# Kernel tuning notes

Hardware: AMD Instinct MI355X
Metric: run time of the kernel (lower is better)

The kernel has to match this reference:

```python
import jax, jax.numpy as jnp
import numpy as np

N_NODES = 20000
N_EDGES = 320000
NFEAT = 50
ALPHA = 0.2  # leaky relu slope
EPS = 1e-16


def _gat_head(x, src, dst, W, a, concat):
    # x: (N, Fin), W: (Fin, Fout), a: (2*Fout,)
    N = x.shape[0]
    Wh = x @ W                      # (N, Fout)
    Fout = W.shape[1]
    # edge_h @ a == Wh[src] @ a[:Fout] + Wh[dst] @ a[Fout:]
    s_src = Wh @ a[:Fout]           # (N,)
    s_dst = Wh @ a[Fout:]           # (N,)
    e = jax.nn.leaky_relu(s_src[src] + s_dst[dst], negative_slope=ALPHA)  # (E,)
    # segment softmax over incoming edges of each target node
    e_max = jax.ops.segment_max(e, dst, num_segments=N)   # (N,)
    e_exp = jnp.exp(e - e_max[dst])                         # (E,)
    e_sum = jax.ops.segment_sum(e_exp, dst, num_segments=N)
    att = e_exp / (e_sum[dst] + EPS)                        # (E,)
    msg = Wh[src] * att[:, None]                            # (E, Fout)
    h = jax.ops.segment_sum(msg, dst, num_segments=N)       # (N, Fout)
    return jax.nn.elu(h) if concat else h


def _multi_head(x, src, dst, W, a, concat):
    # W: (H, Fin, Fout), a: (H, 2*Fout) -> (H, N, Fout)
    return jax.vmap(_gat_head, in_axes=(None, None, None, 0, 0, None))(x, src, dst, W, a, concat)


def setup_inputs() -> dict:
    key = jax.random.key(0)
    ks = jax.random.split(key, 8)
    x = jax.random.normal(ks[0], (N_NODES, NFEAT), dtype=jnp.float32)
    edge_index = jax.random.randint(ks[1], (2, N_EDGES), 0, N_NODES, dtype=jnp.int64)
    s = 0.1
    W1 = jax.random.normal(ks[2], (4, NFEAT, 256), dtype=jnp.float32) * s
    a1 = jax.random.normal(ks[3], (4, 512), dtype=jnp.float32) * s
    W2 = jax.random.normal(ks[4], (4, 1024, 256), dtype=jnp.float32) * s
    a2 = jax.random.normal(ks[5], (4, 512), dtype=jnp.float32) * s
    W3 = jax.random.normal(ks[6], (6, 1024, 121), dtype=jnp.float32) * s
    a3 = jax.random.normal(ks[7], (6, 242), dtype=jnp.float32) * s
    return {"x": x, "edge_index": edge_index, "W1": W1, "a1": a1, "W2": W2, "a2": a2, "W3": W3, "a3": a3}


def reference(x, edge_index, W1, a1, W2, a2, W3, a3):
    src, dst = edge_index[0], edge_index[1]
    N = x.shape[0]
    # layer 1: 4 heads, concat -> (N, 1024), then elu
    h1 = _multi_head(x, src, dst, W1, a1, True)      # (4, N, 256)
    x1 = jnp.transpose(h1, (1, 0, 2)).reshape(N, -1)  # concat along feature dim
    x1 = jax.nn.elu(x1)
    # layer 2: 4 heads, concat + skip connection, then elu
    h2 = _multi_head(x1, src, dst, W2, a2, True)
    x2 = jnp.transpose(h2, (1, 0, 2)).reshape(N, -1)
    x2 = jax.nn.elu(x2 + x1)
    # layer 3: 6 heads, no concat-elu, mean over heads
    h3 = _multi_head(x2, src, dst, W3, a3, False)     # (6, N, 121)
    x3 = jnp.mean(h3, axis=0)
    return jax.nn.sigmoid(x3)
```

## Files before the change

### kernel.cpp

```cpp
#include <hip/hip_runtime.h>
#include <cstdint>

#define N_NODES 20000
#define N_EDGES 320000
#define ALPHA 0.2f
#define GAT_EPS 1e-16f
#define MPAD 20096
#define RBLK 157
#define RHI 20
#define SCAN_BLKS 80
#define BT_ROWS 1152

typedef __attribute__((ext_vector_type(8))) _Float16 half8;
typedef __attribute__((ext_vector_type(4))) _Float16 half4t;
typedef __attribute__((ext_vector_type(16))) float f32x16;
typedef __attribute__((ext_vector_type(2))) float f32x2;

__device__ __forceinline__ float elu1(float x) { return x > 0.f ? x : __expf(x) - 1.f; }

__device__ __forceinline__ unsigned char f2fp8(float x) {
    return (unsigned char)(__builtin_amdgcn_cvt_pk_fp8_f32(x, 0.f, 0, false) & 0xff);
}

__device__ __forceinline__ void async16(const void* g, void* l) {
    __builtin_amdgcn_global_load_lds(
        (const __attribute__((address_space(1))) unsigned int*)g,
        (__attribute__((address_space(3))) unsigned int*)l, 16, 0, 0);
}

__device__ __forceinline__ float rdlanef(float v, int j) {
    return __int_as_float(__builtin_amdgcn_readlane(__float_as_int(v), j));
}

__global__ void hist_kernel(const int* __restrict__ dst, int* __restrict__ counts, int E) {
    int e = blockIdx.x * blockDim.x + threadIdx.x;
    if (e < E) atomicAdd(&counts[dst[e]], 1);
}

__global__ void scan1_kernel(const int* __restrict__ counts, int* __restrict__ excl,
                             int* __restrict__ partial, int N) {
    __shared__ int sh[256];
    int t = threadIdx.x, b = blockIdx.x;
    int i = b * 256 + t;
    int v = (i < N) ? counts[i] : 0;
    sh[t] = v;
    __syncthreads();
    for (int d = 1; d < 256; d <<= 1) {
        int x = (t >= d) ? sh[t - d] : 0;
        __syncthreads();
        sh[t] += x;
        __syncthreads();
    }
    if (i < N) excl[i] = sh[t] - v;
    if (t == 255) partial[b] = sh[255];
}

__global__ void scan2_kernel(int* __restrict__ partial) {
    __shared__ int sh[128];
    int t = threadIdx.x;
    int v = (t < SCAN_BLKS) ? partial[t] : 0;
    sh[t] = v;
    __syncthreads();
    for (int d = 1; d < 128; d <<= 1) {
        int x = (t >= d) ? sh[t - d] : 0;
        __syncthreads();
        sh[t] += x;
        __syncthreads();
    }
    if (t < SCAN_BLKS) partial[t] = sh[t] - v;
}

__global__ void scan3_kernel(const int* __restrict__ excl, const int* __restrict__ partial,
                             int* __restrict__ rowptr, int* __restrict__ cursor, int N, int E) {
    int t = threadIdx.x, b = blockIdx.x;
    int i = b * 256 + t;
    if (i < N) {
        int v = excl[i] + partial[b];
        rowptr[i] = v;
        cursor[i] = v;
    }
    if (i == 0) rowptr[N] = E;
}

__global__ void scatter_kernel(const int* __restrict__ src, const int* __restrict__ dst,
                               int* __restrict__ cursor, int* __restrict__ esrc, int E) {
    int e = blockIdx.x * blockDim.x + threadIdx.x;
    if (e < E) {
        int p = atomicAdd(&cursor[dst[e]], 1);
        esrc[p] = src[e];
    }
}

__global__ void pack_x16(const float* __restrict__ x, _Float16* __restrict__ A) {
    int idx = blockIdx.x * 256 + threadIdx.x;
    int r = idx >> 6, c = idx & 63;
    float v = (r < N_NODES && c < 50) ? x[r * 50 + c] : 0.f;
    A[idx] = (_Float16)v;
}

__global__ void pack_bt1(const float* __restrict__ W, _Float16* __restrict__ Bt) {
    int idx = blockIdx.x * 256 + threadIdx.x;
    int c = idx >> 6, k = idx & 63;
    int h = c >> 8, f = c & 255;
    float v = (k < 50) ? W[((size_t)h * 50 + k) * 256 + f] : 0.f;
    Bt[idx] = (_Float16)v;
}

__global__ void pack_bt16(const float* __restrict__ W, _Float16* __restrict__ Bt,
                          int F, int Fpad, int Ctot) {
    int c = blockIdx.y;
    int k = blockIdx.x * blockDim.x + threadIdx.x;
    float v = 0.f;
    if (c < Ctot) {
        int h = c / Fpad, f = c - h * Fpad;
        if (f < F) v = W[(size_t)h * 1024 * F + (size_t)k * F + f];
    }
    Bt[(size_t)c * 1024 + k] = (_Float16)v;
}

__global__ __launch_bounds__(64) void wtilde_kernel(const float* __restrict__ W,
                                                    const float* __restrict__ a,
                                                    _Float16* __restrict__ BT, int Kreal,
                                                    int Kdim, int F, int H, int Nfeat) {
    int k = blockIdx.x, j = blockIdx.y;
    if (j >= 2 * H) return;
    int lane = threadIdx.x;
    int h = j < H ? j : j - H;
    int ao = j < H ? 0 : F;
    float s = 0.f;
    if (k < Kreal) {
        const float* wp = W + ((size_t)h * Kreal + k) * F;
        const float* ap = a + (size_t)h * 2 * F + ao;
        for (int f = lane; f < F; f += 64) s += wp[f] * ap[f];
    }
#pragma unroll
    for (int off = 32; off; off >>= 1) s += __shfl_down(s, off);
    if (lane == 0) BT[(size_t)(Nfeat + j) * Kdim + k] = (_Float16)s;
}

__global__ __launch_bounds__(256) void gemm_f16(const _Float16* __restrict__ A,
                                                const _Float16* __restrict__ BT,
                                                unsigned char* __restrict__ C8,
                                                float* __restrict__ SPRE,
                                                int M, int Nfeat, int ld, int Kdim, int Cblk) {
    int id = blockIdx.x;
    int xm = id & 7, q = id >> 3;
    int cb = q % Cblk, rh = q / Cblk;
    int rb = rh * 8 + xm;
    if (rb >= RBLK) return;
    __shared__ __align__(16) _Float16 sA[128 * 64];
    __shared__ __align__(16) _Float16 sB[128 * 64];
    int t = threadIdx.x;
    int row0 = rb * 128, col0 = cb * 128;
    int lane = t & 63, wave = t >> 6;
    int wm = wave >> 1, wn = wave & 1;
    int l31 = lane & 31;
    int lhi = lane >> 5;

    const _Float16* gA = A + (size_t)row0 * Kdim;
    const _Float16* gB = BT + (size_t)col0 * Kdim;

    int sR[4], sgl[4];
#pragma unroll
    for (int i = 0; i < 4; i++) {
        int m = i * 256 + t;
        sR[i] = m >> 3;
        sgl[i] = (m & 7) ^ (sR[i] & 7);
    }

    f32x16 acc[2][2] = {};

    for (int k0 = 0; k0 < Kdim; k0 += 64) {
        __syncthreads();
#pragma unroll
        for (int i = 0; i < 4; i++) {
            const _Float16* pa = gA + (size_t)sR[i] * Kdim + k0 + sgl[i] * 8;
            const _Float16* pb = gB + (size_t)sR[i] * Kdim + k0 + sgl[i] * 8;
            async16(pa, sA + (i * 256 + t) * 8);
            async16(pb, sB + (i * 256 + t) * 8);
        }
        __syncthreads();
#pragma unroll
        for (int kk = 0; kk < 4; kk++) {
            int g = kk * 2 + lhi;
            half8 af[2], bf[2];
#pragma unroll
            for (int mt = 0; mt < 2; mt++) {
                int R = wm * 64 + mt * 32 + l31;
                int gp = g ^ (R & 7);
                af[mt] = *(const half8*)(sA + R * 64 + gp * 8);
            }
#pragma unroll
            for (int nt = 0; nt < 2; nt++) {
                int R = wn * 64 + nt * 32 + l31;
                int gp = g ^ (R & 7);
                bf[nt] = *(const half8*)(sB + R * 64 + gp * 8);
            }
#pragma unroll
            for (int mt = 0; mt < 2; mt++)
#pragma unroll
                for (int nt = 0; nt < 2; nt++)
                    acc[mt][nt] = __builtin_amdgcn_mfma_f32_32x32x16_f16(af[mt], bf[nt], acc[mt][nt], 0, 0, 0);
        }
    }

    int cb32 = col0 + wn * 64 + l31;
    int rb32 = row0 + wm * 64 + 4 * lhi;
#pragma unroll
    for (int mt = 0; mt < 2; mt++)
#pragma unroll
        for (int nt = 0; nt < 2; nt++) {
            int gc = cb32 + nt * 32;
            if (gc < Nfeat) {
#pragma unroll
                for (int r = 0; r < 16; r++) {
                    int gr = rb32 + mt * 32 + (r & 3) + 8 * (r >> 2);
                    if (gr < M) C8[(size_t)gr * ld + gc] = f2fp8(acc[mt][nt][r]);
                }
            } else if (gc < Nfeat + 12) {
                int j = gc - Nfeat;
#pragma unroll
                for (int r = 0; r < 16; r++) {
                    int gr = rb32 + mt * 32 + (r & 3) + 8 * (r >> 2);
                    if (gr < M) SPRE[(size_t)j * N_NODES + gr] = acc[mt][nt][r];
                }
            }
        }
}

__global__ __launch_bounds__(256) void attagg256_kernel(const int* __restrict__ rowptr,
                                                        const int* __restrict__ esrc,
                                                        const float* __restrict__ SPRE,
                                                        const unsigned char* __restrict__ WH8,
                                                        _Float16* __restrict__ X16,
                                                        int use_skip, int N) {
    int n = blockIdx.x;
    int h = threadIdx.x >> 6;
    int lane = threadIdx.x & 63;
    int start = rowptr[n], end = rowptr[n + 1];
    int cnt = end - start;
    const float* ss = SPRE + (size_t)h * N;
    float sd = SPRE[(size_t)(4 + h) * N + n];
    const unsigned char* Wb = WH8 + h * 256 + lane * 4;
    float a0 = 0.f, a1 = 0.f, a2 = 0.f, a3 = 0.f;

    if (cnt <= 64) {
        int e = start + lane;
        bool act = e < end;
        int idx = act ? esrc[e] : 0;

        unsigned int wA[8], wB[8], wC[8], wD[8];
        auto ISSUE = [&](unsigned int (&buf)[8], int base) {
#pragma unroll
            for (int u = 0; u < 8; u++) {
                int ij = __builtin_amdgcn_readlane(idx, base + u);
                buf[u] = *(const unsigned int*)(Wb + ((size_t)(unsigned)ij << 10));
            }
        };
        ISSUE(wA, 0);
        if (cnt > 8)  ISSUE(wB, 8);
        if (cnt > 16) ISSUE(wC, 16);
        if (cnt > 24) ISSUE(wD, 24);

        float sc = -1e30f;
        if (act) {
            sc = ss[idx] + sd;
            sc = sc > 0.f ? sc : ALPHA * sc;
        }
        float m = sc;
#pragma unroll
        for (int off = 1; off < 64; off <<= 1) m = fmaxf(m, __shfl_xor(m, off));
        float ptil = act ? __expf(sc - m) : 0.f;
        float s = ptil;
#pragma unroll
        for (int off = 1; off < 64; off <<= 1) s += __shfl_xor(s, off);
        float p = ptil * (1.f / (s + GAT_EPS));

        auto CONSUME = [&](unsigned int (&buf)[8], int base) {
#pragma unroll
            for (int u = 0; u < 8; u++) {
                float pj = rdlanef(p, base + u);
                f32x2 lo = __builtin_amdgcn_cvt_pk_f32_fp8((int)buf[u], false);
                f32x2 hi = __builtin_amdgcn_cvt_pk_f32_fp8((int)buf[u], true);
                a0 += pj * lo.x; a1 += pj * lo.y; a2 += pj * hi.x; a3 += pj * hi.y;
            }
        };
        CONSUME(wA, 0);
        if (cnt > 8)  { if (cnt > 32) ISSUE(wA, 32); CONSUME(wB, 8); }
        if (cnt > 16) { if (cnt > 40) ISSUE(wB, 40); CONSUME(wC, 16); }
        if (cnt > 24) { if (cnt > 48) ISSUE(wC, 48); CONSUME(wD, 24); }
        if (cnt > 32) { if (cnt > 56) ISSUE(wD, 56); CONSUME(wA, 32); }
        if (cnt > 40) CONSUME(wB, 40);
        if (cnt > 48) CONSUME(wC, 48);
        if (cnt > 56) CONSUME(wD, 56);
    } else {
        float m = -1e30f, s = 0.f;
        int sidx = 0; float ssc = -1e30f;
        for (int e0 = start; e0 < end; e0 += 64) {
            int e = e0 + lane;
            bool act = e < end;
            int idx = act ? esrc[e] : 0;
            float sc = -1e30f;
            if (act) {
                sc = ss[idx] + sd;
                sc = sc > 0.f ? sc : ALPHA * sc;
            }
            sidx = idx; ssc = sc;
            float mn = fmaxf(m, sc);
            s = s * __expf(m - mn) + (act ? __expf(sc - mn) : 0.f);
            m = mn;
        }
        float lm = m;
#pragma unroll
        for (int off = 1; off < 64; off <<= 1) m = fmaxf(m, __shfl_xor(m, off));
        float ptil = s * __expf(lm - m);
        s = ptil;
#pragma unroll
        for (int off = 1; off < 64; off <<= 1) s += __shfl_xor(s, off);
        float inv = 1.f / (s + GAT_EPS);

        int lastStart = start + (((end - start - 1) >> 6) << 6);
        for (int e0 = start; e0 < end; e0 += 64) {
            int e = e0 + lane;
            bool act = e < end;
            int idx; float p;
            if (e0 == lastStart) {
                idx = sidx;
                p = act ? __expf(ssc - m) * inv : 0.f;
            } else {
                idx = act ? esrc[e] : 0;
                float sc = -1e30f;
                if (act) {
                    sc = ss[idx] + sd;
                    sc = sc > 0.f ? sc : ALPHA * sc;
                }
                p = act ? __expf(sc - m) * inv : 0.f;
            }
            int cn = end - e0; if (cn > 64) cn = 64;
            int j = 0;
            for (; j + 4 <= cn; j += 4) {
                int i0 = __builtin_amdgcn_readlane(idx, j);
                int i1 = __builtin_amdgcn_readlane(idx, j + 1);
                int i2 = __builtin_amdgcn_readlane(idx, j + 2);
                int i3 = __builtin_amdgcn_readlane(idx, j + 3);
                float p0 = rdlanef(p, j), p1 = rdlanef(p, j + 1);
                float p2 = rdlanef(p, j + 2), p3 = rdlanef(p, j + 3);
                unsigned int w0 = *(const unsigned int*)(Wb + (size_t)i0 * 1024);
                unsigned int w1 = *(const unsigned int*)(Wb + (size_t)i1 * 1024);
                unsigned int w2 = *(const unsigned int*)(Wb + (size_t)i2 * 1024);
                unsigned int w3 = *(const unsigned int*)(Wb + (size_t)i3 * 1024);
                f32x2 l0 = __builtin_amdgcn_cvt_pk_f32_fp8((int)w0, false);
                f32x2 h0v = __builtin_amdgcn_cvt_pk_f32_fp8((int)w0, true);
                f32x2 l1 = __builtin_amdgcn_cvt_pk_f32_fp8((int)w1, false);
                f32x2 h1v = __builtin_amdgcn_cvt_pk_f32_fp8((int)w1, true);
                f32x2 l2 = __builtin_amdgcn_cvt_pk_f32_fp8((int)w2, false);
                f32x2 h2v = __builtin_amdgcn_cvt_pk_f32_fp8((int)w2, true);
                f32x2 l3 = __builtin_amdgcn_cvt_pk_f32_fp8((int)w3, false);
                f32x2 h3v = __builtin_amdgcn_cvt_pk_f32_fp8((int)w3, true);
                a0 += p0 * l0.x + p1 * l1.x + p2 * l2.x + p3 * l3.x;
                a1 += p0 * l0.y + p1 * l1.y + p2 * l2.y + p3 * l3.y;
                a2 += p0 * h0v.x + p1 * h1v.x + p2 * h2v.x + p3 * h3v.x;
                a3 += p0 * h0v.y + p1 * h1v.y + p2 * h2v.y + p3 * h3v.y;
            }
            for (; j < cn; j++) {
                int ij = __builtin_amdgcn_readlane(idx, j);
                float pj = rdlanef(p, j);
                unsigned int w = *(const unsigned int*)(Wb + (size_t)ij * 1024);
                f32x2 lo = __builtin_amdgcn_cvt_pk_f32_fp8((int)w, false);
                f32x2 hi = __builtin_amdgcn_cvt_pk_f32_fp8((int)w, true);
                a0 += pj * lo.x; a1 += pj * lo.y; a2 += pj * hi.x; a3 += pj * hi.y;
            }
        }
    }

    size_t o = (size_t)n * 1024 + h * 256 + lane * 4;
    float v0, v1, v2, v3;
    if (use_skip) {
        half4t sk = *(const half4t*)(X16 + o);
        v0 = elu1(elu1(a0) + (float)sk.x);
        v1 = elu1(elu1(a1) + (float)sk.y);
        v2 = elu1(elu1(a2) + (float)sk.z);
        v3 = elu1(elu1(a3) + (float)sk.w);
    } else {
        v0 = elu1(elu1(a0)); v1 = elu1(elu1(a1));
        v2 = elu1(elu1(a2)); v3 = elu1(elu1(a3));
    }
    half4t r;
    r.x = (_Float16)v0; r.y = (_Float16)v1; r.z = (_Float16)v2; r.w = (_Float16)v3;
    *(half4t*)(X16 + o) = r;
}

__global__ __launch_bounds__(384) void attagg726_kernel(const int* __restrict__ rowptr,
                                                        const int* __restrict__ esrc,
                                                        const float* __restrict__ SPRE,
                                                        const unsigned char* __restrict__ WH8,
                                                        float* __restrict__ out, int N) {
    __shared__ float part[6][124];
    int n = blockIdx.x;
    int t = threadIdx.x;
    int h = t >> 6;
    int lane = t & 63;
    int start = rowptr[n], end = rowptr[n + 1];
    int cnt = end - start;
    const float* ss = SPRE + (size_t)h * N;
    float sd = SPRE[(size_t)(6 + h) * N + n];
    const unsigned char* Wb = WH8 + h * 124 + 2 * lane;
    float a0 = 0.f, a1 = 0.f;

    if (cnt <= 64) {
        int e = start + lane;
        bool act = e < end;
        int idx = act ? esrc[e] : 0;

        unsigned short wA[8], wB[8], wC[8], wD[8];
        auto ISSUE = [&](unsigned short (&buf)[8], int base) {
#pragma unroll
            for (int u = 0; u < 8; u++) {
                int ij = __builtin_amdgcn_readlane(idx, base + u);
                buf[u] = *(const unsigned short*)(Wb + (size_t)(unsigned)ij * 768u);
            }
        };
        ISSUE(wA, 0);
        if (cnt > 8)  ISSUE(wB, 8);
        if (cnt > 16) ISSUE(wC, 16);
        if (cnt > 24) ISSUE(wD, 24);

        float sc = -1e30f;
        if (act) {
            sc = ss[idx] + sd;
            sc = sc > 0.f ? sc : ALPHA * sc;
        }
        float m = sc;
#pragma unroll
        for (int off = 1; off < 64; off <<= 1) m = fmaxf(m, __shfl_xor(m, off));
        float ptil = act ? __expf(sc - m) : 0.f;
        float s = ptil;
#pragma unroll
        for (int off = 1; off < 64; off <<= 1) s += __shfl_xor(s, off);
        float p = ptil * (1.f / (s + GAT_EPS));

        auto CONSUME = [&](unsigned short (&buf)[8], int base) {
#pragma unroll
            for (int u = 0; u < 8; u++) {
                float pj = rdlanef(p, base + u);
                f32x2 f = __builtin_amdgcn_cvt_pk_f32_fp8((int)buf[u], false);
                a0 += pj * f.x; a1 += pj * f.y;
            }
        };
        CONSUME(wA, 0);
        if (cnt > 8)  { if (cnt > 32) ISSUE(wA, 32); CONSUME(wB, 8); }
        if (cnt > 16) { if (cnt > 40) ISSUE(wB, 40); CONSUME(wC, 16); }
        if (cnt > 24) { if (cnt > 48) ISSUE(wC, 48); CONSUME(wD, 24); }
        if (cnt > 32) { if (cnt > 56) ISSUE(wD, 56); CONSUME(wA, 32); }
        if (cnt > 40) CONSUME(wB, 40);
        if (cnt > 48) CONSUME(wC, 48);
        if (cnt > 56) CONSUME(wD, 56);
    } else {
        float m = -1e30f, s = 0.f;
        int sidx = 0; float ssc = -1e30f;
        for (int e0 = start; e0 < end; e0 += 64) {
            int e = e0 + lane;
            bool act = e < end;
            int idx = act ? esrc[e] : 0;
            float sc = -1e30f;
            if (act) {
                sc = ss[idx] + sd;
                sc = sc > 0.f ? sc : ALPHA * sc;
            }
            sidx = idx; ssc = sc;
            float mn = fmaxf(m, sc);
            s = s * __expf(m - mn) + (act ? __expf(sc - mn) : 0.f);
            m = mn;
        }
        float lm = m;
#pragma unroll
        for (int off = 1; off < 64; off <<= 1) m = fmaxf(m, __shfl_xor(m, off));
        float ptil = s * __expf(lm - m);
        s = ptil;
#pragma unroll
        for (int off = 1; off < 64; off <<= 1) s += __shfl_xor(s, off);
        float inv = 1.f / (s + GAT_EPS);

        int lastStart = start + (((end - start - 1) >> 6) << 6);
        for (int e0 = start; e0 < end; e0 += 64) {
            int e = e0 + lane;
            bool act = e < end;
            int idx; float p;
            if (e0 == lastStart) {
                idx = sidx;
                p = act ? __expf(ssc - m) * inv : 0.f;
            } else {
                idx = act ? esrc[e] : 0;
                float sc = -1e30f;
                if (act) {
                    sc = ss[idx] + sd;
                    sc = sc > 0.f ? sc : ALPHA * sc;
                }
                p = act ? __expf(sc - m) * inv : 0.f;
            }
            int cn = end - e0; if (cn > 64) cn = 64;
            int j = 0;
            for (; j + 4 <= cn; j += 4) {
                int i0 = __builtin_amdgcn_readlane(idx, j);
                int i1 = __builtin_amdgcn_readlane(idx, j + 1);
                int i2 = __builtin_amdgcn_readlane(idx, j + 2);
                int i3 = __builtin_amdgcn_readlane(idx, j + 3);
                float p0 = rdlanef(p, j), p1 = rdlanef(p, j + 1);
                float p2 = rdlanef(p, j + 2), p3 = rdlanef(p, j + 3);
                unsigned short w0 = *(const unsigned short*)(Wb + (size_t)i0 * 768);
                unsigned short w1 = *(const unsigned short*)(Wb + (size_t)i1 * 768);
                unsigned short w2 = *(const unsigned short*)(Wb + (size_t)i2 * 768);
                unsigned short w3 = *(const unsigned short*)(Wb + (size_t)i3 * 768);
                f32x2 f0 = __builtin_amdgcn_cvt_pk_f32_fp8((int)w0, false);
                f32x2 f1 = __builtin_amdgcn_cvt_pk_f32_fp8((int)w1, false);
                f32x2 f2 = __builtin_amdgcn_cvt_pk_f32_fp8((int)w2, false);
                f32x2 f3 = __builtin_amdgcn_cvt_pk_f32_fp8((int)w3, false);
                a0 += p0 * f0.x + p1 * f1.x + p2 * f2.x + p3 * f3.x;
                a1 += p0 * f0.y + p1 * f1.y + p2 * f2.y + p3 * f3.y;
            }
            for (; j < cn; j++) {
                int ij = __builtin_amdgcn_readlane(idx, j);
                float pj = rdlanef(p, j);
                unsigned short w = *(const unsigned short*)(Wb + (size_t)ij * 768);
                f32x2 f = __builtin_amdgcn_cvt_pk_f32_fp8((int)w, false);
                a0 += pj * f.x; a1 += pj * f.y;
            }
        }
    }

    if (lane < 62) {
        part[h][2 * lane]     = a0;
        part[h][2 * lane + 1] = a1;
    }
    __syncthreads();
    if (t < 121) {
        float tot = (part[0][t] + part[1][t] + part[2][t] +
                     part[3][t] + part[4][t] + part[5][t]) * (1.f / 6.f);
        out[(size_t)n * 121 + t] = 1.f / (1.f + __expf(-tot));
    }
}

extern "C" void kernel_launch(void* const* d_in, const int* in_sizes, int n_in,
                              void* d_out, int out_size, void* d_ws, size_t ws_size,
                              hipStream_t stream) {
    const float* x  = (const float*)d_in[0];
    const int*   ei = (const int*)d_in[1];
    const float* W1 = (const float*)d_in[2];
    const float* a1 = (const float*)d_in[3];
    const float* W2 = (const float*)d_in[4];
    const float* a2 = (const float*)d_in[5];
    const float* W3 = (const float*)d_in[6];
    const float* a3 = (const float*)d_in[7];
    float* out = (float*)d_out;
    const int N = N_NODES, E = N_EDGES;
    const int* src = ei;
    const int* dst = ei + E;

    char* ws = (char*)d_ws;
    size_t off = 0;
    auto alloc = [&](size_t b) { size_t o = off; off += (b + 255) & ~(size_t)255; return o; };
    _Float16* X16  = (_Float16*)(ws + alloc((size_t)MPAD * 1024 * 2));
    unsigned char* WH8 = (unsigned char*)(ws + alloc((size_t)MPAD * 1024));
    _Float16* BT16 = (_Float16*)(ws + alloc((size_t)BT_ROWS * 1024 * 2));
    _Float16* A1   = (_Float16*)(ws + alloc((size_t)MPAD * 64 * 2));
    _Float16* BT1  = (_Float16*)(ws + alloc((size_t)BT_ROWS * 64 * 2));
    float* SPRE   = (float*)(ws + alloc((size_t)12 * N * 4));
    int*   rowptr = (int*)(ws + alloc((size_t)(N + 1) * 4));
    int*   cursor = (int*)(ws + alloc((size_t)N * 4));
    int*   counts = (int*)(ws + alloc((size_t)N * 4));
    int*   excl   = (int*)(ws + alloc((size_t)N * 4));
    int*   partial= (int*)(ws + alloc((size_t)SCAN_BLKS * 4));
    int*   esrc   = (int*)(ws + alloc((size_t)E * 4));

    hipMemsetAsync(counts, 0, (size_t)N * 4, stream);
    hist_kernel<<<(E + 255) / 256, 256, 0, stream>>>(dst, counts, E);
    scan1_kernel<<<SCAN_BLKS, 256, 0, stream>>>(counts, excl, partial, N);
    scan2_kernel<<<1, 128, 0, stream>>>(partial);
    scan3_kernel<<<SCAN_BLKS, 256, 0, stream>>>(excl, partial, rowptr, cursor, N, E);
    scatter_kernel<<<(E + 255) / 256, 256, 0, stream>>>(src, dst, cursor, esrc, E);
    hipMemsetAsync(X16 + (size_t)N * 1024, 0, (size_t)(MPAD - N) * 1024 * 2, stream);

    pack_x16<<<MPAD * 64 / 256, 256, 0, stream>>>(x, A1);
    pack_bt1<<<1024 * 64 / 256, 256, 0, stream>>>(W1, BT1);
    wtilde_kernel<<<dim3(64, 8), 64, 0, stream>>>(W1, a1, BT1, 50, 64, 256, 4, 1024);
    gemm_f16<<<8 * RHI * 9, 256, 0, stream>>>(A1, BT1, WH8, SPRE, N, 1024, 1024, 64, 9);
    attagg256_kernel<<<N, 256, 0, stream>>>(rowptr, esrc, SPRE, WH8, X16, 0, N);

    pack_bt16<<<dim3(4, 1024), 256, 0, stream>>>(W2, BT16, 256, 256, 1024);
    wtilde_kernel<<<dim3(1024, 8), 64, 0, stream>>>(W2, a2, BT16, 1024, 1024, 256, 4, 1024);
    gemm_f16<<<8 * RHI * 9, 256, 0, stream>>>(X16, BT16, WH8, SPRE, N, 1024, 1024, 1024, 9);
    attagg256_kernel<<<N, 256, 0, stream>>>(rowptr, esrc, SPRE, WH8, X16, 1, N);

    pack_bt16<<<dim3(4, 744), 256, 0, stream>>>(W3, BT16, 121, 124, 744);
    wtilde_kernel<<<dim3(1024, 12), 64, 0, stream>>>(W3, a3, BT16, 1024, 1024, 121, 6, 744);
    gemm_f16<<<8 * RHI * 6, 256, 0, stream>>>(X16, BT16, WH8, SPRE, N, 744, 768, 1024, 6);
    attagg726_kernel<<<N, 384, 0, stream>>>(rowptr, esrc, SPRE, WH8, out, N);
}
```

Baseline: 444.5 us.

## Aggregate raw input features before projection in layer one (reassociate GEMM)

Layer one now computes only the attention scores with a small GEMM, then aggregates the 64-wide fp16 input rows per head (aggx1) instead of gathering 1024-wide fp8 projected rows. A second GEMM multiplies the aggregated features by W1 per head, using a per-column-block K offset, and applies the double ELU in its epilogue, writing fp16 X16 directly. This cuts layer-one gather traffic and the fp8 round-trip of Wh. In exchange it adds an extra GEMM launch, a new 256-wide intermediate buffer, and a changed precision path.

```diff
diff --git a/kernel.cpp b/kernel.cpp
--- a/kernel.cpp
+++ b/kernel.cpp
@@ -142,7 +142,8 @@
                                                 const _Float16* __restrict__ BT,
                                                 unsigned char* __restrict__ C8,
                                                 float* __restrict__ SPRE,
-                                                int M, int Nfeat, int ld, int Kdim, int Cblk) {
+                                                int M, int Nfeat, int ld, int Kdim, int Cblk,
+                                                int ldA, int mode) {
     int id = blockIdx.x;
     int xm = id & 7, q = id >> 3;
     int cb = q % Cblk, rh = q / Cblk;
@@ -157,7 +158,8 @@
     int l31 = lane & 31;
     int lhi = lane >> 5;
 
-    const _Float16* gA = A + (size_t)row0 * Kdim;
+    int koff = (mode == 1) ? ((cb >> 1) * 64) : 0;
+    const _Float16* gA = A + (size_t)row0 * ldA + koff;
     const _Float16* gB = BT + (size_t)col0 * Kdim;
 
     int sR[4], sgl[4];
@@ -174,7 +176,7 @@
         __syncthreads();
 #pragma unroll
         for (int i = 0; i < 4; i++) {
-            const _Float16* pa = gA + (size_t)sR[i] * Kdim + k0 + sgl[i] * 8;
+            const _Float16* pa = gA + (size_t)sR[i] * ldA + k0 + sgl[i] * 8;
             const _Float16* pb = gB + (size_t)sR[i] * Kdim + k0 + sgl[i] * 8;
             async16(pa, sA + (i * 256 + t) * 8);
             async16(pb, sB + (i * 256 + t) * 8);
@@ -206,6 +208,23 @@
 
     int cb32 = col0 + wn * 64 + l31;
     int rb32 = row0 + wm * 64 + 4 * lhi;
+    if (mode == 1) {
+        _Float16* C16 = (_Float16*)C8;
+#pragma unroll
+        for (int mt = 0; mt < 2; mt++)
+#pragma unroll
+            for (int nt = 0; nt < 2; nt++) {
+                int gc = cb32 + nt * 32;
+                if (gc < Nfeat) {
+#pragma unroll
+                    for (int r = 0; r < 16; r++) {
+                        int gr = rb32 + mt * 32 + (r & 3) + 8 * (r >> 2);
+                        if (gr < M) C16[(size_t)gr * ld + gc] = (_Float16)elu1(elu1(acc[mt][nt][r]));
+                    }
+                }
+            }
+        return;
+    }
 #pragma unroll
     for (int mt = 0; mt < 2; mt++)
 #pragma unroll
@@ -228,12 +247,11 @@
         }
 }
 
-__global__ __launch_bounds__(256) void attagg256_kernel(const int* __restrict__ rowptr,
-                                                        const int* __restrict__ esrc,
-                                                        const float* __restrict__ SPRE,
-                                                        const unsigned char* __restrict__ WH8,
-                                                        _Float16* __restrict__ X16,
-                                                        int use_skip, int N) {
+__global__ __launch_bounds__(256) void aggx1_kernel(const int* __restrict__ rowptr,
+                                                    const int* __restrict__ esrc,
+                                                    const float* __restrict__ SPRE,
+                                                    const _Float16* __restrict__ A1,
+                                                    _Float16* __restrict__ XB, int N) {
     int n = blockIdx.x;
     int h = threadIdx.x >> 6;
     int lane = threadIdx.x & 63;
@@ -241,20 +259,21 @@
     int cnt = end - start;
     const float* ss = SPRE + (size_t)h * N;
     float sd = SPRE[(size_t)(4 + h) * N + n];
-    const unsigned char* Wb = WH8 + h * 256 + lane * 4;
-    float a0 = 0.f, a1 = 0.f, a2 = 0.f, a3 = 0.f;
+    const unsigned char* Wb = (const unsigned char*)A1 + 2 * lane;
+    float acc = 0.f;
 
     if (cnt <= 64) {
         int e = start + lane;
         bool act = e < end;
         int idx = act ? esrc[e] : 0;
-
-        unsigned int wA[8], wB[8], wC[8], wD[8];
-        auto ISSUE = [&](unsigned int (&buf)[8], int base) {
+        int voff = idx << 7;
+
+        unsigned short wA[8], wB[8], wC[8], wD[8];
+        auto ISSUE = [&](unsigned short (&buf)[8], int base) {
 #pragma unroll
             for (int u = 0; u < 8; u++) {
-                int ij = __builtin_amdgcn_readlane(idx, base + u);
-                buf[u] = *(const unsigned int*)(Wb + ((size_t)(unsigned)ij << 10));
+                int off = __builtin_amdgcn_readlane(voff, base + u);
+                buf[u] = *(const unsigned short*)(Wb + (unsigned)off);
             }
         };
         ISSUE(wA, 0);
@@ -276,13 +295,11 @@
         for (int off = 1; off < 64; off <<= 1) s += __shfl_xor(s, off);
         float p = ptil * (1.f / (s + GAT_EPS));
 
-        auto CONSUME = [&](unsigned int (&buf)[8], int base) {
+        auto CONSUME = [&](unsigned short (&buf)[8], int base) {
 #pragma unroll
             for (int u = 0; u < 8; u++) {
                 float pj = rdlanef(p, base + u);
-                f32x2 lo = __builtin_amdgcn_cvt_pk_f32_fp8((int)buf[u], false);
-                f32x2 hi = __builtin_amdgcn_cvt_pk_f32_fp8((int)buf[u], true);
-                a0 += pj * lo.x; a1 += pj * lo.y; a2 += pj * hi.x; a3 += pj * hi.y;
+                acc += pj * (float)(*(const _Float16*)&buf[u]);
             }
         };
         CONSUME(wA, 0);
@@ -337,87 +354,45 @@
                 p = act ? __expf(sc - m) * inv : 0.f;
             }
             int cn = end - e0; if (cn > 64) cn = 64;
-            int j = 0;
-            for (; j + 4 <= cn; j += 4) {
-                int i0 = __builtin_amdgcn_readlane(idx, j);
-                int i1 = __builtin_amdgcn_readlane(idx, j + 1);
-                int i2 = __builtin_amdgcn_readlane(idx, j + 2);
-                int i3 = __builtin_amdgcn_readlane(idx, j + 3);
-                float p0 = rdlanef(p, j), p1 = rdlanef(p, j + 1);
-                float p2 = rdlanef(p, j + 2), p3 = rdlanef(p, j + 3);
-                unsigned int w0 = *(const unsigned int*)(Wb + (size_t)i0 * 1024);
-                unsigned int w1 = *(const unsigned int*)(Wb + (size_t)i1 * 1024);
-                unsigned int w2 = *(const unsigned int*)(Wb + (size_t)i2 * 1024);
-                unsigned int w3 = *(const unsigned int*)(Wb + (size_t)i3 * 1024);
-                f32x2 l0 = __builtin_amdgcn_cvt_pk_f32_fp8((int)w0, false);
-                f32x2 h0v = __builtin_amdgcn_cvt_pk_f32_fp8((int)w0, true);
-                f32x2 l1 = __builtin_amdgcn_cvt_pk_f32_fp8((int)w1, false);
-                f32x2 h1v = __builtin_amdgcn_cvt_pk_f32_fp8((int)w1, true);
-                f32x2 l2 = __builtin_amdgcn_cvt_pk_f32_fp8((int)w2, false);
-                f32x2 h2v = __builtin_amdgcn_cvt_pk_f32_fp8((int)w2, true);
-                f32x2 l3 = __builtin_amdgcn_cvt_pk_f32_fp8((int)w3, false);
-                f32x2 h3v = __builtin_amdgcn_cvt_pk_f32_fp8((int)w3, true);
-                a0 += p0 * l0.x + p1 * l1.x + p2 * l2.x + p3 * l3.x;
-                a1 += p0 * l0.y + p1 * l1.y + p2 * l2.y + p3 * l3.y;
-                a2 += p0 * h0v.x + p1 * h1v.x + p2 * h2v.x + p3 * h3v.x;
-                a3 += p0 * h0v.y + p1 * h1v.y + p2 * h2v.y + p3 * h3v.y;
-            }
-            for (; j < cn; j++) {
+            for (int j = 0; j < cn; j++) {
                 int ij = __builtin_amdgcn_readlane(idx, j);
                 float pj = rdlanef(p, j);
-                unsigned int w = *(const unsigned int*)(Wb + (size_t)ij * 1024);
-                f32x2 lo = __builtin_amdgcn_cvt_pk_f32_fp8((int)w, false);
-                f32x2 hi = __builtin_amdgcn_cvt_pk_f32_fp8((int)w, true);
-                a0 += pj * lo.x; a1 += pj * lo.y; a2 += pj * hi.x; a3 += pj * hi.y;
-            }
-        }
-    }
-
-    size_t o = (size_t)n * 1024 + h * 256 + lane * 4;
-    float v0, v1, v2, v3;
-    if (use_skip) {
-        half4t sk = *(const half4t*)(X16 + o);
-        v0 = elu1(elu1(a0) + (float)sk.x);
-        v1 = elu1(elu1(a1) + (float)sk.y);
-        v2 = elu1(elu1(a2) + (float)sk.z);
-        v3 = elu1(elu1(a3) + (float)sk.w);
-    } else {
-        v0 = elu1(elu1(a0)); v1 = elu1(elu1(a1));
-        v2 = elu1(elu1(a2)); v3 = elu1(elu1(a3));
-    }
-    half4t r;
-    r.x = (_Float16)v0; r.y = (_Float16)v1; r.z = (_Float16)v2; r.w = (_Float16)v3;
-    *(half4t*)(X16 + o) = r;
-}
-
-__global__ __launch_bounds__(384) void attagg726_kernel(const int* __restrict__ rowptr,
+                unsigned short w = *(const unsigned short*)(Wb + ((size_t)(unsigned)ij << 7));
+                acc += pj * (float)(*(const _Float16*)&w);
+            }
+        }
+    }
+
+    XB[(size_t)n * 256 + h * 64 + lane] = (_Float16)acc;
+}
+
+__global__ __launch_bounds__(256) void attagg256_kernel(const int* __restrict__ rowptr,
                                                         const int* __restrict__ esrc,
                                                         const float* __restrict__ SPRE,
                                                         const unsigned char* __restrict__ WH8,
-                                                        float* __restrict__ out, int N) {
-    __shared__ float part[6][124];
+                                                        _Float16* __restrict__ X16,
+                                                        int use_skip, int N) {
     int n = blockIdx.x;
-    int t = threadIdx.x;
-    int h = t >> 6;
-    int lane = t & 63;
+    int h = threadIdx.x >> 6;
+    int lane = threadIdx.x & 63;
     int start = rowptr[n], end = rowptr[n + 1];
     int cnt = end - start;
     const float* ss = SPRE + (size_t)h * N;
-    float sd = SPRE[(size_t)(6 + h) * N + n];
-    const unsigned char* Wb = WH8 + h * 124 + 2 * lane;
-    float a0 = 0.f, a1 = 0.f;
+    float sd = SPRE[(size_t)(4 + h) * N + n];
+    const unsigned char* Wb = WH8 + h * 256 + lane * 4;
+    float a0 = 0.f, a1 = 0.f, a2 = 0.f, a3 = 0.f;
 
     if (cnt <= 64) {
         int e = start + lane;
         bool act = e < end;
         int idx = act ? esrc[e] : 0;
 
-        unsigned short wA[8], wB[8], wC[8], wD[8];
-        auto ISSUE = [&](unsigned short (&buf)[8], int base) {
+        unsigned int wA[8], wB[8], wC[8], wD[8];
+        auto ISSUE = [&](unsigned int (&buf)[8], int base) {
 #pragma unroll
             for (int u = 0; u < 8; u++) {
                 int ij = __builtin_amdgcn_readlane(idx, base + u);
-                buf[u] = *(const unsigned short*)(Wb + (size_t)(unsigned)ij * 768u);
+                buf[u] = *(const unsigned int*)(Wb + ((size_t)(unsigned)ij << 10));
             }
         };
         ISSUE(wA, 0);
@@ -439,12 +414,13 @@
         for (int off = 1; off < 64; off <<= 1) s += __shfl_xor(s, off);
         float p = ptil * (1.f / (s + GAT_EPS));
 
-        auto CONSUME = [&](unsigned short (&buf)[8], int base) {
+        auto CONSUME = [&](unsigned int (&buf)[8], int base) {
 #pragma unroll
             for (int u = 0; u < 8; u++) {
                 float pj = rdlanef(p, base + u);
-                f32x2 f = __builtin_amdgcn_cvt_pk_f32_fp8((int)buf[u], false);
-                a0 += pj * f.x; a1 += pj * f.y;
+                f32x2 lo = __builtin_amdgcn_cvt_pk_f32_fp8((int)buf[u], false);
+                f32x2 hi = __builtin_amdgcn_cvt_pk_f32_fp8((int)buf[u], true);
+                a0 += pj * lo.x; a1 += pj * lo.y; a2 += pj * hi.x; a3 += pj * hi.y;
             }
         };
         CONSUME(wA, 0);
@@ -499,26 +475,144 @@
                 p = act ? __expf(sc - m) * inv : 0.f;
             }
             int cn = end - e0; if (cn > 64) cn = 64;
-            int j = 0;
-            for (; j + 4 <= cn; j += 4) {
-                int i0 = __builtin_amdgcn_readlane(idx, j);
-                int i1 = __builtin_amdgcn_readlane(idx, j + 1);
-                int i2 = __builtin_amdgcn_readlane(idx, j + 2);
-                int i3 = __builtin_amdgcn_readlane(idx, j + 3);
-                float p0 = rdlanef(p, j), p1 = rdlanef(p, j + 1);
-                float p2 = rdlanef(p, j + 2), p3 = rdlanef(p, j + 3);
-                unsigned short w0 = *(const unsigned short*)(Wb + (size_t)i0 * 768);
-                unsigned short w1 = *(const unsigned short*)(Wb + (size_t)i1 * 768);
-                unsigned short w2 = *(const unsigned short*)(Wb + (size_t)i2 * 768);
-                unsigned short w3 = *(const unsigned short*)(Wb + (size_t)i3 * 768);
-                f32x2 f0 = __builtin_amdgcn_cvt_pk_f32_fp8((int)w0, false);
-                f32x2 f1 = __builtin_amdgcn_cvt_pk_f32_fp8((int)w1, false);
-                f32x2 f2 = __builtin_amdgcn_cvt_pk_f32_fp8((int)w2, false);
-                f32x2 f3 = __builtin_amdgcn_cvt_pk_f32_fp8((int)w3, false);
-                a0 += p0 * f0.x + p1 * f1.x + p2 * f2.x + p3 * f3.x;
-                a1 += p0 * f0.y + p1 * f1.y + p2 * f2.y + p3 * f3.y;
-            }
-            for (; j < cn; j++) {
+            for (int j = 0; j < cn; j++) {
+                int ij = __builtin_amdgcn_readlane(idx, j);
+                float pj = rdlanef(p, j);
+                unsigned int w = *(const unsigned int*)(Wb + (size_t)ij * 1024);
+                f32x2 lo = __builtin_amdgcn_cvt_pk_f32_fp8((int)w, false);
+                f32x2 hi = __builtin_amdgcn_cvt_pk_f32_fp8((int)w, true);
+                a0 += pj * lo.x; a1 += pj * lo.y; a2 += pj * hi.x; a3 += pj * hi.y;
+            }
+        }
+    }
+
+    size_t o = (size_t)n * 1024 + h * 256 + lane * 4;
+    float v0, v1, v2, v3;
+    if (use_skip) {
+        half4t sk = *(const half4t*)(X16 + o);
+        v0 = elu1(elu1(a0) + (float)sk.x);
+        v1 = elu1(elu1(a1) + (float)sk.y);
+        v2 = elu1(elu1(a2) + (float)sk.z);
+        v3 = elu1(elu1(a3) + (float)sk.w);
+    } else {
+        v0 = elu1(elu1(a0)); v1 = elu1(elu1(a1));
+        v2 = elu1(elu1(a2)); v3 = elu1(elu1(a3));
+    }
+    half4t r;
+    r.x = (_Float16)v0; r.y = (_Float16)v1; r.z = (_Float16)v2; r.w = (_Float16)v3;
+    *(half4t*)(X16 + o) = r;
+}
+
+__global__ __launch_bounds__(384) void attagg726_kernel(const int* __restrict__ rowptr,
+                                                        const int* __restrict__ esrc,
+                                                        const float* __restrict__ SPRE,
+                                                        const unsigned char* __restrict__ WH8,
+                                                        float* __restrict__ out, int N) {
+    __shared__ float part[6][124];
+    int n = blockIdx.x;
+    int t = threadIdx.x;
+    int h = t >> 6;
+    int lane = t & 63;
+    int start = rowptr[n], end = rowptr[n + 1];
+    int cnt = end - start;
+    const float* ss = SPRE + (size_t)h * N;
+    float sd = SPRE[(size_t)(6 + h) * N + n];
+    const unsigned char* Wb = WH8 + h * 124 + 2 * lane;
+    float a0 = 0.f, a1 = 0.f;
+
+    if (cnt <= 64) {
+        int e = start + lane;
+        bool act = e < end;
+        int idx = act ? esrc[e] : 0;
+
+        unsigned short wA[8], wB[8], wC[8], wD[8];
+        auto ISSUE = [&](unsigned short (&buf)[8], int base) {
+#pragma unroll
+            for (int u = 0; u < 8; u++) {
+                int ij = __builtin_amdgcn_readlane(idx, base + u);
+                buf[u] = *(const unsigned short*)(Wb + (size_t)(unsigned)ij * 768u);
+            }
+        };
+        ISSUE(wA, 0);
+        if (cnt > 8)  ISSUE(wB, 8);
+        if (cnt > 16) ISSUE(wC, 16);
+        if (cnt > 24) ISSUE(wD, 24);
+
+        float sc = -1e30f;
+        if (act) {
+            sc = ss[idx] + sd;
+            sc = sc > 0.f ? sc : ALPHA * sc;
+        }
+        float m = sc;
+#pragma unroll
+        for (int off = 1; off < 64; off <<= 1) m = fmaxf(m, __shfl_xor(m, off));
+        float ptil = act ? __expf(sc - m) : 0.f;
+        float s = ptil;
+#pragma unroll
+        for (int off = 1; off < 64; off <<= 1) s += __shfl_xor(s, off);
+        float p = ptil * (1.f / (s + GAT_EPS));
+
+        auto CONSUME = [&](unsigned short (&buf)[8], int base) {
+#pragma unroll
+            for (int u = 0; u < 8; u++) {
+                float pj = rdlanef(p, base + u);
+                f32x2 f = __builtin_amdgcn_cvt_pk_f32_fp8((int)buf[u], false);
+                a0 += pj * f.x; a1 += pj * f.y;
+            }
+        };
+        CONSUME(wA, 0);
+        if (cnt > 8)  { if (cnt > 32) ISSUE(wA, 32); CONSUME(wB, 8); }
+        if (cnt > 16) { if (cnt > 40) ISSUE(wB, 40); CONSUME(wC, 16); }
+        if (cnt > 24) { if (cnt > 48) ISSUE(wC, 48); CONSUME(wD, 24); }
+        if (cnt > 32) { if (cnt > 56) ISSUE(wD, 56); CONSUME(wA, 32); }
+        if (cnt > 40) CONSUME(wB, 40);
+        if (cnt > 48) CONSUME(wC, 48);
+        if (cnt > 56) CONSUME(wD, 56);
+    } else {
+        float m = -1e30f, s = 0.f;
+        int sidx = 0; float ssc = -1e30f;
+        for (int e0 = start; e0 < end; e0 += 64) {
+            int e = e0 + lane;
+            bool act = e < end;
+            int idx = act ? esrc[e] : 0;
+            float sc = -1e30f;
+            if (act) {
+                sc = ss[idx] + sd;
+                sc = sc > 0.f ? sc : ALPHA * sc;
+            }
+            sidx = idx; ssc = sc;
+            float mn = fmaxf(m, sc);
+            s = s * __expf(m - mn) + (act ? __expf(sc - mn) : 0.f);
+            m = mn;
+        }
+        float lm = m;
+#pragma unroll
+        for (int off = 1; off < 64; off <<= 1) m = fmaxf(m, __shfl_xor(m, off));
+        float ptil = s * __expf(lm - m);
+        s = ptil;
+#pragma unroll
+        for (int off = 1; off < 64; off <<= 1) s += __shfl_xor(s, off);
+        float inv = 1.f / (s + GAT_EPS);
+
+        int lastStart = start + (((end - start - 1) >> 6) << 6);
+        for (int e0 = start; e0 < end; e0 += 64) {
+            int e = e0 + lane;
+            bool act = e < end;
+            int idx; float p;
+            if (e0 == lastStart) {
+                idx = sidx;
+                p = act ? __expf(ssc - m) * inv : 0.f;
+            } else {
+                idx = act ? esrc[e] : 0;
+                float sc = -1e30f;
+                if (act) {
+                    sc = ss[idx] + sd;
+                    sc = sc > 0.f ? sc : ALPHA * sc;
+                }
+                p = act ? __expf(sc - m) * inv : 0.f;
+            }
+            int cn = end - e0; if (cn > 64) cn = 64;
+            for (int j = 0; j < cn; j++) {
                 int ij = __builtin_amdgcn_readlane(idx, j);
                 float pj = rdlanef(p, j);
                 unsigned short w = *(const unsigned short*)(Wb + (size_t)ij * 768);
@@ -564,6 +658,8 @@
     _Float16* BT16 = (_Float16*)(ws + alloc((size_t)BT_ROWS * 1024 * 2));
     _Float16* A1   = (_Float16*)(ws + alloc((size_t)MPAD * 64 * 2));
     _Float16* BT1  = (_Float16*)(ws + alloc((size_t)BT_ROWS * 64 * 2));
+    _Float16* XB   = (_Float16*)(ws + alloc((size_t)MPAD * 256 * 2));
+    _Float16* BTS  = (_Float16*)(ws + alloc((size_t)128 * 64 * 2));
     float* SPRE   = (float*)(ws + alloc((size_t)12 * N * 4));
     int*   rowptr = (int*)(ws + alloc((size_t)(N + 1) * 4));
     int*   cursor = (int*)(ws + alloc((size_t)N * 4));
@@ -579,20 +675,22 @@
     scan3_kernel<<<SCAN_BLKS, 256, 0, stream>>>(excl, partial, rowptr, cursor, N, E);
     scatter_kernel<<<(E + 255) / 256, 256, 0, stream>>>(src, dst, cursor, esrc, E);
     hipMemsetAsync(X16 + (size_t)N * 1024, 0, (size_t)(MPAD - N) * 1024 * 2, stream);
+    hipMemsetAsync(XB + (size_t)N * 256, 0, (size_t)(MPAD - N) * 256 * 2, stream);
 
     pack_x16<<<MPAD * 64 / 256, 256, 0, stream>>>(x, A1);
     pack_bt1<<<1024 * 64 / 256, 256, 0, stream>>>(W1, BT1);
-    wtilde_kernel<<<dim3(64, 8), 64, 0, stream>>>(W1, a1, BT1, 50, 64, 256, 4, 1024);
-    gemm_f16<<<8 * RHI * 9, 256, 0, stream>>>(A1, BT1, WH8, SPRE, N, 1024, 1024, 64, 9);
-    attagg256_kernel<<<N, 256, 0, stream>>>(rowptr, esrc, SPRE, WH8, X16, 0, N);
+    wtilde_kernel<<<dim3(64, 8), 64, 0, stream>>>(W1, a1, BTS, 50, 64, 256, 4, 0);
+    gemm_f16<<<8 * RHI * 1, 256, 0, stream>>>(A1, BTS, WH8, SPRE, N, 0, 1024, 64, 1, 64, 0);
+    aggx1_kernel<<<N, 256, 0, stream>>>(rowptr, esrc, SPRE, A1, XB, N);
+    gemm_f16<<<8 * RHI * 8, 256, 0, stream>>>(XB, BT1, (unsigned char*)X16, SPRE, N, 1024, 1024, 64, 8, 256, 1);
 
     pack_bt16<<<dim3(4, 1024), 256, 0, stream>>>(W2, BT16, 256, 256, 1024);
     wtilde_kernel<<<dim3(1024, 8), 64, 0, stream>>>(W2, a2, BT16, 1024, 1024, 256, 4, 1024);
-    gemm_f16<<<8 * RHI * 9, 256, 0, stream>>>(X16, BT16, WH8, SPRE, N, 1024, 1024, 1024, 9);
+    gemm_f16<<<8 * RHI * 9, 256, 0, stream>>>(X16, BT16, WH8, SPRE, N, 1024, 1024, 1024, 9, 1024, 0);
     attagg256_kernel<<<N, 256, 0, stream>>>(rowptr, esrc, SPRE, WH8, X16, 1, N);
 
     pack_bt16<<<dim3(4, 744), 256, 0, stream>>>(W3, BT16, 121, 124, 744);
     wtilde_kernel<<<dim3(1024, 12), 64, 0, stream>>>(W3, a3, BT16, 1024, 1024, 121, 6, 744);
-    gemm_f16<<<8 * RHI * 6, 256, 0, stream>>>(X16, BT16, WH8, SPRE, N, 744, 768, 1024, 6);
+    gemm_f16<<<8 * RHI * 6, 256, 0, stream>>>(X16, BT16, WH8, SPRE, N, 744, 768, 1024, 6, 1024, 0);
     attagg726_kernel<<<N, 384, 0, stream>>>(rowptr, esrc, SPRE, WH8, out, N);
 }
```

Result: faster. 434.2 us (-2.3%).
